# Optimization experiments

Measured on AMD Instinct MI355X. Metric: run time of the kernel, lower is better.

## Reference

```python
import jax, jax.numpy as jnp
import numpy as np

N_EMB = 256
HEAD_SIZE = 64
B, S = 4, 4096


def setup_inputs() -> dict:
    key = jax.random.key(0)
    k1, k2, k3, k4 = jax.random.split(key, 4)
    return {
        "ini_emb": jax.random.normal(k1, (B, S, N_EMB), dtype=jnp.float32),
        "wk": jax.random.normal(k2, (N_EMB, HEAD_SIZE), dtype=jnp.float32) * (N_EMB ** -0.5),
        "wq": jax.random.normal(k3, (N_EMB, HEAD_SIZE), dtype=jnp.float32) * (N_EMB ** -0.5),
        "wv": jax.random.normal(k4, (N_EMB, HEAD_SIZE), dtype=jnp.float32) * (N_EMB ** -0.5),
    }


def reference(ini_emb, wk, wq, wv):
    # projections: [B,S,E] @ [E,H] -> [B,S,H]
    k = ini_emb @ wk
    q = ini_emb @ wq
    v = ini_emb @ wv
    # scores: [B,S,S]; NOTE: source scales by n_emb**-0.5, not head_size**-0.5
    scores = jnp.einsum("bqh,bkh->bqk", q, k) * (N_EMB ** -0.5)
    attn = jax.nn.softmax(scores, axis=-1)
    # output: [B,S,H]
    return jnp.einsum("bqk,bkh->bqh", attn, v)
```

## Files before the change

kernel.cpp:

```cpp
#include <hip/hip_runtime.h>


typedef short short4v __attribute__((ext_vector_type(4)));
typedef short short8v __attribute__((ext_vector_type(8)));
typedef float floatx4 __attribute__((ext_vector_type(4)));
typedef unsigned short u16;
typedef unsigned int u32;

#define SEQ 4096
#define EMB 256
#define HD 64
#define PADA 264

static __device__ __forceinline__ u16 f2bf(float x) {
    union { float f; unsigned u; } v; v.f = x;
    unsigned r = v.u + 0x7FFFu + ((v.u >> 16) & 1u);
    return (u16)(r >> 16);
}

static __device__ __forceinline__ u32 cvt_pk_bf16(float a, float b) {
    u32 r;
    asm("v_cvt_pk_bf16_f32 %0, %1, %2" : "=v"(r) : "v"(a), "v"(b));
    return r;
}

static __device__ __forceinline__ short4v pack_bf4(float a, float b, float c, float d) {
    union { u32 u[2]; short4v s; } x;
    x.u[0] = cvt_pk_bf16(a, b);
    x.u[1] = cvt_pk_bf16(c, d);
    return x.s;
}

__global__ __launch_bounds__(256) void prep_w(
    const float* __restrict__ wk, const float* __restrict__ wq, const float* __restrict__ wv,
    u16* __restrict__ wt) {
    const int nt = blockIdx.x;
    const int t = threadIdx.x;
#pragma unroll
    for (int ss = 0; ss < 2; ++ss) {
        int slot = t + ss * 256;
        int kc = slot >> 6, lane = slot & 63;
        int ln15 = lane & 15, lq = lane >> 4;
        int cg = nt * 16 + ln15;
        int mat = cg >> 6, col = cg & 63;
        const float* W = (mat == 0) ? wq : (mat == 1) ? wk : wv;
        const float s = (mat == 0) ? 0.0625f * 1.44269504088896f : 1.0f;
        u32 w4[4];
#pragma unroll
        for (int p = 0; p < 2; ++p) {
#pragma unroll
            for (int d = 0; d < 2; ++d) {
                int e0 = kc * 32 + lq * 8 + p * 4 + d * 2;
                u16 lo = f2bf(W[(e0 + 0) * HD + col] * s);
                u16 hi = f2bf(W[(e0 + 1) * HD + col] * s);
                w4[p * 2 + d] = (u32)lo | ((u32)hi << 16);
            }
        }
        u32* dst = (u32*)wt + ((size_t)(nt * 8 + kc) * 64 + lane) * 4;
        *(uint4*)dst = make_uint4(w4[0], w4[1], w4[2], w4[3]);
    }
}

__global__ __launch_bounds__(256) void proj_mfma(
    const float* __restrict__ emb, const u16* __restrict__ wt,
    u16* __restrict__ qb, u16* __restrict__ kb, u16* __restrict__ vbt) {
    __shared__ u16 a_s[16 * PADA];
    const int t = threadIdx.x;
    const int lane = t & 63;
    const int wave = t >> 6;
    const int ln15 = lane & 15;
    const int lq = lane >> 4;
    const size_t row0 = (size_t)blockIdx.x * 16;

#pragma unroll
    for (int c = 0; c < 4; ++c) {
        int f = t + c * 256;
        int row = f >> 6, e4 = (f & 63) * 4;
        float4 v = *(const float4*)(emb + (row0 + row) * EMB + e4);
        u32 lo = cvt_pk_bf16(v.x, v.y);
        u32 hi = cvt_pk_bf16(v.z, v.w);
        *(uint2*)&a_s[row * PADA + e4] = make_uint2(lo, hi);
    }
    __syncthreads();

    floatx4 acc[3];
#pragma unroll
    for (int j = 0; j < 3; ++j) {
        floatx4 z = { 0.f, 0.f, 0.f, 0.f };
        acc[j] = z;
    }

#pragma unroll
    for (int kc = 0; kc < 8; ++kc) {
        short8v a = *(const short8v*)&a_s[ln15 * PADA + kc * 32 + lq * 8];
#pragma unroll
        for (int j = 0; j < 3; ++j) {
            short8v b = *(const short8v*)(wt + (((size_t)(wave * 3 + j) * 8 + kc) * 64 + lane) * 8);
            acc[j] = __builtin_amdgcn_mfma_f32_16x16x32_bf16(a, b, acc[j], 0, 0, 0);
        }
    }

#pragma unroll
    for (int j = 0; j < 3; ++j) {
        int cg = (wave * 3 + j) * 16 + ln15;
        int mat = cg >> 6, col = cg & 63;
        if (mat < 2) {
            u16* O = (mat == 0) ? qb : kb;
#pragma unroll
            for (int r = 0; r < 4; ++r)
                O[(row0 + lq * 4 + r) * HD + col] = f2bf(acc[j][r]);
        } else {
            u32 lo = cvt_pk_bf16(acc[j][0], acc[j][1]);
            u32 hi = cvt_pk_bf16(acc[j][2], acc[j][3]);
            size_t bidx = row0 >> 12;
            size_t sl = (row0 & 4095) + lq * 4;
            *(uint2*)&vbt[(bidx * 64 + col) * SEQ + sl] = make_uint2(lo, hi);
        }
    }
}


__global__ __launch_bounds__(256) void attn_kernel(
    const u16* __restrict__ qb, const u16* __restrict__ kb, const u16* __restrict__ vbt,
    float* __restrict__ po, float* __restrict__ pml) {
    __shared__ __align__(16) u16 smem[4][64 * 64];

    const int t = threadIdx.x;
    const int lane = t & 63;
    const int wave = t >> 6;
    const int ln15 = lane & 15;
    const int lq = lane >> 4;

    const int part = ((blockIdx.x & 7) << 6) | (blockIdx.x >> 3);
    const int b = part >> 7;
    const int qblk = (part >> 2) & 31;
    const int split = part & 3;
    const int q0 = qblk * 128;

    const u16* __restrict__ qpb = qb + ((size_t)b * SEQ + q0) * HD;
    const u16* __restrict__ kpb = kb + (size_t)b * SEQ * HD;
    const u16* __restrict__ vpb = vbt + (size_t)b * HD * SEQ;

    short8v qf[2][2];
#pragma unroll
    for (int nt = 0; nt < 2; ++nt)
#pragma unroll
        for (int h = 0; h < 2; ++h)
            qf[nt][h] = *(const short8v*)(qpb + (size_t)(wave * 32 + nt * 16 + ln15) * HD + h * 32 + lq * 8);

    floatx4 oacc[4][2];
#pragma unroll
    for (int ht = 0; ht < 4; ++ht)
#pragma unroll
        for (int nt = 0; nt < 2; ++nt) {
            floatx4 z = { 0.f, 0.f, 0.f, 0.f };
            oacc[ht][nt] = z;
        }
    float lacc[2] = { 0.f, 0.f };

    const int r0 = t >> 3, c0 = t & 7, r1 = r0 + 32;
    const int sw0 = r0 * 64 + ((c0 ^ (r0 & 7)) * 8);
    const int sw1 = r1 * 64 + ((c0 ^ (r1 & 7)) * 8);

    const int xk = ln15 & 7;
    const int ksw_lo = ln15 * 64 + ((lq ^ xk) * 8);
    const int ksw_hi = ln15 * 64 + (((4 + lq) ^ xk) * 8);
    const int vch0 = lq >> 1, vsub = (lq & 1) * 4;

    uint4 ka, kb4, va, vb4;
    {
        const int kwb = (split * 16) * 64;
        ka  = *(const uint4*)(kpb + (size_t)(kwb + r0) * HD + c0 * 8);
        kb4 = *(const uint4*)(kpb + (size_t)(kwb + r1) * HD + c0 * 8);
        va  = *(const uint4*)(vpb + (size_t)r0 * SEQ + kwb + c0 * 8);
        vb4 = *(const uint4*)(vpb + (size_t)r1 * SEQ + kwb + c0 * 8);
        *(uint4*)(&smem[0][0] + sw0) = ka;
        *(uint4*)(&smem[0][0] + sw1) = kb4;
        *(uint4*)(&smem[1][0] + sw0) = va;
        *(uint4*)(&smem[1][0] + sw1) = vb4;
    }
    __syncthreads();

#pragma unroll 1
    for (int tt = 0; tt < 16; ++tt) {
        const int buf = tt & 1;
        if (tt < 15) {
            const int kwb = (split * 16 + tt + 1) * 64;
            ka  = *(const uint4*)(kpb + (size_t)(kwb + r0) * HD + c0 * 8);
            kb4 = *(const uint4*)(kpb + (size_t)(kwb + r1) * HD + c0 * 8);
            va  = *(const uint4*)(vpb + (size_t)r0 * SEQ + kwb + c0 * 8);
            vb4 = *(const uint4*)(vpb + (size_t)r1 * SEQ + kwb + c0 * 8);
        }

        const u16* ktp = &smem[buf * 2 + 0][0];
        const u16* vtp = &smem[buf * 2 + 1][0];

#pragma unroll
        for (int kt = 0; kt < 4; ++kt) {
            short8v k0 = *(const short8v*)(ktp + kt * 1024 + ksw_lo);
            short8v k1 = *(const short8v*)(ktp + kt * 1024 + ksw_hi);

            floatx4 s[2];
            __builtin_amdgcn_s_setprio(1);
#pragma unroll
            for (int nt = 0; nt < 2; ++nt) {
                floatx4 z = { 0.f, 0.f, 0.f, 0.f };
                s[nt] = __builtin_amdgcn_mfma_f32_16x16x32_bf16(k0, qf[nt][0], z, 0, 0, 0);
                s[nt] = __builtin_amdgcn_mfma_f32_16x16x32_bf16(k1, qf[nt][1], s[nt], 0, 0, 0);
            }
            __builtin_amdgcn_s_setprio(0);

            short4v pf[2];
#pragma unroll
            for (int nt = 0; nt < 2; ++nt) {
                float p0 = __builtin_amdgcn_exp2f(s[nt][0]);
                float p1 = __builtin_amdgcn_exp2f(s[nt][1]);
                float p2 = __builtin_amdgcn_exp2f(s[nt][2]);
                float p3 = __builtin_amdgcn_exp2f(s[nt][3]);
                lacc[nt] += (p0 + p1) + (p2 + p3);
                pf[nt] = pack_bf4(p0, p1, p2, p3);
            }

            __builtin_amdgcn_s_setprio(1);
#pragma unroll
            for (int ht = 0; ht < 4; ++ht) {
                short4v vf = *(const short4v*)(vtp + ht * 1024 + ln15 * 64
                               + (((kt * 2 + vch0) ^ xk) * 8) + vsub);
#pragma unroll
                for (int nt = 0; nt < 2; ++nt)
                    oacc[ht][nt] = __builtin_amdgcn_mfma_f32_16x16x16bf16_1k(
                        vf, pf[nt], oacc[ht][nt], 0, 0, 0);
            }
            __builtin_amdgcn_s_setprio(0);
        }

        if (tt < 15) {
            u16* ktn = &smem[(buf ^ 1) * 2 + 0][0];
            u16* vtn = &smem[(buf ^ 1) * 2 + 1][0];
            *(uint4*)(ktn + sw0) = ka;
            *(uint4*)(ktn + sw1) = kb4;
            *(uint4*)(vtn + sw0) = va;
            *(uint4*)(vtn + sw1) = vb4;
        }
        __syncthreads();
    }

#pragma unroll
    for (int nt = 0; nt < 2; ++nt) {
        lacc[nt] += __shfl_xor(lacc[nt], 16);
        lacc[nt] += __shfl_xor(lacc[nt], 32);
    }
    if (lq == 0) {
#pragma unroll
        for (int nt = 0; nt < 2; ++nt)
            pml[(size_t)part * 128 + wave * 32 + nt * 16 + ln15] = lacc[nt];
    }

    float* __restrict__ pob = po + (size_t)part * 8192;
#pragma unroll
    for (int ht = 0; ht < 4; ++ht)
#pragma unroll
        for (int nt = 0; nt < 2; ++nt)
            *(floatx4*)&pob[(wave * 32 + nt * 16 + ln15) * 64 + ht * 16 + lq * 4] = oacc[ht][nt];
}

__global__ __launch_bounds__(256) void reduce_kernel(
    const float* __restrict__ po, const float* __restrict__ pml,
    float* __restrict__ out) {
    __shared__ float ls[128];
    const int t = threadIdx.x;
    const int bq = blockIdx.x >> 1;
    const int half = blockIdx.x & 1;
    const int part0 = bq * 4;

    if (t < 128)
        ls[t] = pml[(size_t)(part0 + 0) * 128 + t] + pml[(size_t)(part0 + 1) * 128 + t]
              + pml[(size_t)(part0 + 2) * 128 + t] + pml[(size_t)(part0 + 3) * 128 + t];
    __syncthreads();

    const float* __restrict__ p0 = po + (size_t)(part0 + 0) * 8192;
    const float* __restrict__ p1 = po + (size_t)(part0 + 1) * 8192;
    const float* __restrict__ p2 = po + (size_t)(part0 + 2) * 8192;
    const float* __restrict__ p3 = po + (size_t)(part0 + 3) * 8192;
    float* __restrict__ ob = out + ((size_t)(bq >> 5) * SEQ + (size_t)(bq & 31) * 128) * HD;

#pragma unroll
    for (int i = 0; i < 4; ++i) {
        int f4 = half * 1024 + t + i * 256;
        int f = f4 * 4;
        int q = f4 >> 4;
        float4 a = *(const float4*)&p0[f];
        float4 c = *(const float4*)&p1[f];
        float4 d = *(const float4*)&p2[f];
        float4 e = *(const float4*)&p3[f];
        float inv = 1.0f / ls[q];
        float4 r;
        r.x = (a.x + c.x + d.x + e.x) * inv;
        r.y = (a.y + c.y + d.y + e.y) * inv;
        r.z = (a.z + c.z + d.z + e.z) * inv;
        r.w = (a.w + c.w + d.w + e.w) * inv;
        *(float4*)&ob[f] = r;
    }
}

extern "C" void kernel_launch(void* const* d_in, const int* in_sizes, int n_in,
                              void* d_out, int out_size, void* d_ws, size_t ws_size,
                              hipStream_t stream) {
    const float* emb = (const float*)d_in[0];
    const float* wk  = (const float*)d_in[1];
    const float* wq  = (const float*)d_in[2];
    const float* wv  = (const float*)d_in[3];

    u16* qb  = (u16*)d_ws;
    u16* kb  = (u16*)((char*)d_ws + (size_t)2 * 1024 * 1024);
    u16* vbt = (u16*)((char*)d_ws + (size_t)4 * 1024 * 1024);
    u16* wt  = (u16*)((char*)d_ws + (size_t)6 * 1024 * 1024);
    float* po  = (float*)((char*)d_ws + (size_t)6 * 1024 * 1024 + 256 * 1024);
    float* pml = (float*)((char*)d_ws + (size_t)22 * 1024 * 1024 + 256 * 1024);
    float* out = (float*)d_out;

    prep_w<<<12, 256, 0, stream>>>(wk, wq, wv, wt);
    proj_mfma<<<1024, 256, 0, stream>>>(emb, wt, qb, kb, vbt);
    attn_kernel<<<512, 256, 0, stream>>>(qb, kb, vbt, po, pml);
    reduce_kernel<<<256, 256, 0, stream>>>(po, pml, out);
}
```

Before: 114.7 us.

## Process 32 rows per projection block and stage outputs in LDS for coalesced stores

The projection kernel now handles 32 rows per block instead of 16, so each weight fragment loaded from global memory feeds two MFMAs. Grid size is halved to match. Results are staged in a shared-memory tile and then written with 16-byte coalesced stores for Q, K and the transposed V, replacing scattered 2-byte and 8-byte stores. This adds an extra barrier and shared-memory traffic, and the transposed gather reads from LDS with strided access.

```diff
diff --git a/kernel.cpp b/kernel.cpp
--- a/kernel.cpp
+++ b/kernel.cpp
@@ -3,6 +3,7 @@
 
 typedef short short4v __attribute__((ext_vector_type(4)));
 typedef short short8v __attribute__((ext_vector_type(8)));
+typedef unsigned short ushort8v __attribute__((ext_vector_type(8)));
 typedef float floatx4 __attribute__((ext_vector_type(4)));
 typedef unsigned short u16;
 typedef unsigned int u32;
@@ -64,16 +65,17 @@
 __global__ __launch_bounds__(256) void proj_mfma(
     const float* __restrict__ emb, const u16* __restrict__ wt,
     u16* __restrict__ qb, u16* __restrict__ kb, u16* __restrict__ vbt) {
-    __shared__ u16 a_s[16 * PADA];
+    __shared__ u16 a_s[32 * PADA];
+    __shared__ __align__(16) u16 ot_s[12][32][16];
     const int t = threadIdx.x;
     const int lane = t & 63;
     const int wave = t >> 6;
     const int ln15 = lane & 15;
     const int lq = lane >> 4;
-    const size_t row0 = (size_t)blockIdx.x * 16;
-
-#pragma unroll
-    for (int c = 0; c < 4; ++c) {
+    const size_t row0 = (size_t)blockIdx.x * 32;
+
+#pragma unroll
+    for (int c = 0; c < 8; ++c) {
         int f = t + c * 256;
         int row = f >> 6, e4 = (f & 63) * 4;
         float4 v = *(const float4*)(emb + (row0 + row) * EMB + e4);
@@ -83,39 +85,54 @@
     }
     __syncthreads();
 
-    floatx4 acc[3];
-#pragma unroll
-    for (int j = 0; j < 3; ++j) {
-        floatx4 z = { 0.f, 0.f, 0.f, 0.f };
-        acc[j] = z;
-    }
+    floatx4 acc[2][3];
+#pragma unroll
+    for (int rg = 0; rg < 2; ++rg)
+#pragma unroll
+        for (int j = 0; j < 3; ++j) {
+            floatx4 z = { 0.f, 0.f, 0.f, 0.f };
+            acc[rg][j] = z;
+        }
 
 #pragma unroll
     for (int kc = 0; kc < 8; ++kc) {
-        short8v a = *(const short8v*)&a_s[ln15 * PADA + kc * 32 + lq * 8];
+        short8v a0 = *(const short8v*)&a_s[ln15 * PADA + kc * 32 + lq * 8];
+        short8v a1 = *(const short8v*)&a_s[(16 + ln15) * PADA + kc * 32 + lq * 8];
 #pragma unroll
         for (int j = 0; j < 3; ++j) {
             short8v b = *(const short8v*)(wt + (((size_t)(wave * 3 + j) * 8 + kc) * 64 + lane) * 8);
-            acc[j] = __builtin_amdgcn_mfma_f32_16x16x32_bf16(a, b, acc[j], 0, 0, 0);
-        }
-    }
-
-#pragma unroll
-    for (int j = 0; j < 3; ++j) {
-        int cg = (wave * 3 + j) * 16 + ln15;
-        int mat = cg >> 6, col = cg & 63;
-        if (mat < 2) {
-            u16* O = (mat == 0) ? qb : kb;
+            acc[0][j] = __builtin_amdgcn_mfma_f32_16x16x32_bf16(a0, b, acc[0][j], 0, 0, 0);
+            acc[1][j] = __builtin_amdgcn_mfma_f32_16x16x32_bf16(a1, b, acc[1][j], 0, 0, 0);
+        }
+    }
+
+#pragma unroll
+    for (int rg = 0; rg < 2; ++rg)
+#pragma unroll
+        for (int j = 0; j < 3; ++j)
 #pragma unroll
             for (int r = 0; r < 4; ++r)
-                O[(row0 + lq * 4 + r) * HD + col] = f2bf(acc[j][r]);
-        } else {
-            u32 lo = cvt_pk_bf16(acc[j][0], acc[j][1]);
-            u32 hi = cvt_pk_bf16(acc[j][2], acc[j][3]);
-            size_t bidx = row0 >> 12;
-            size_t sl = (row0 & 4095) + lq * 4;
-            *(uint2*)&vbt[(bidx * 64 + col) * SEQ + sl] = make_uint2(lo, hi);
-        }
+                ot_s[wave * 3 + j][rg * 16 + lq * 4 + r][ln15] = f2bf(acc[rg][j][r]);
+    __syncthreads();
+
+    {
+        const int row = t >> 3, chunk = t & 7;
+        const int tile = chunk >> 1, off = (chunk & 1) * 8;
+        ushort8v qv = *(const ushort8v*)&ot_s[tile][row][off];
+        *(ushort8v*)&qb[(row0 + row) * HD + chunk * 8] = qv;
+        ushort8v kv = *(const ushort8v*)&ot_s[4 + tile][row][off];
+        *(ushort8v*)&kb[(row0 + row) * HD + chunk * 8] = kv;
+    }
+    {
+        const int h = t >> 2, sc = t & 3;
+        const int tile = 8 + (h >> 4), tcol = h & 15;
+        union { u16 u[8]; ushort8v v; } g;
+#pragma unroll
+        for (int i = 0; i < 8; ++i)
+            g.u[i] = ot_s[tile][sc * 8 + i][tcol];
+        size_t bidx = row0 >> 12;
+        size_t sl = (row0 & 4095) + sc * 8;
+        *(ushort8v*)&vbt[(bidx * 64 + h) * SEQ + sl] = g.v;
     }
 }
 
@@ -320,7 +337,7 @@
     float* out = (float*)d_out;
 
     prep_w<<<12, 256, 0, stream>>>(wk, wq, wv, wt);
-    proj_mfma<<<1024, 256, 0, stream>>>(emb, wt, qb, kb, vbt);
+    proj_mfma<<<512, 256, 0, stream>>>(emb, wt, qb, kb, vbt);
     attn_kernel<<<512, 256, 0, stream>>>(qb, kb, vbt, po, pml);
     reduce_kernel<<<256, 256, 0, stream>>>(po, pml, out);
 }
```

New measurement: 112.3 us, median of 2. 1.02x faster.
